# Optimization experiments

Hardware: AMD Instinct MI355X
Metric: run time of the kernel (lower is better)

## Reference

```python
import jax, jax.numpy as jnp
import numpy as np

VOCAB_SIZES = [100003, 100019, 100043, 100049, 100057, 100069, 100103, 100109,
               100129, 100151, 100153, 100169, 100183, 100189, 100193, 100207]
OFFSETS = np.cumsum([0] + VOCAB_SIZES[:-1]).astype(np.int32)  # per-head offsets into shared table
B, S, G, C = 2, 2048, 4, 2048        # batch, seq, hc_mult branches, base_emb_dim
H, DH = 16, 64                        # total hash heads, dim_per_head
ENGRAM_DIM = H * DH                   # 1024 = num_orders * dim_per_ngram
K, DIL = 4, 3                         # conv kernel_size, dilation = max_ngram_size


def setup_inputs() -> dict:
  key = jax.random.key(0)
  ks = jax.random.split(key, 8)
  total_vocab = sum(VOCAB_SIZES)
  return {
      "hidden_states": jax.random.normal(ks[0], (B, S, G, C), jnp.float32),
      "hash_input_ids": jax.random.randint(ks[1], (B, S, H), 0, min(VOCAB_SIZES), jnp.int32),
      "emb_table": jax.random.normal(ks[2], (total_vocab, DH), jnp.float32) * 0.02,
      "key_w": jax.random.normal(ks[3], (G, ENGRAM_DIM, C), jnp.float32) / np.sqrt(ENGRAM_DIM),
      "key_b": jnp.zeros((G, C), jnp.float32),
      "k_scale": jnp.ones((G, C), jnp.float32) + 0.02 * jax.random.normal(ks[4], (G, C), jnp.float32),
      "q_scale": jnp.ones((G, C), jnp.float32) + 0.02 * jax.random.normal(ks[5], (G, C), jnp.float32),
      "value_w": jax.random.normal(ks[6], (ENGRAM_DIM, C), jnp.float32) / np.sqrt(ENGRAM_DIM),
      "value_b": jnp.zeros((C,), jnp.float32),
      "conv_scale": jnp.ones((G, C), jnp.float32),
      "conv_w": jax.random.normal(ks[7], (K, G * C), jnp.float32) * 0.25,  # depthwise taps
  }


def _rmsnorm(x, scale, eps):
  var = jnp.mean(jnp.square(x), axis=-1, keepdims=True)
  return x * jax.lax.rsqrt(var + eps) * scale


def reference(hidden_states, hash_input_ids, emb_table, key_w, key_b,
              k_scale, q_scale, value_w, value_b, conv_scale, conv_w):
  # 1. Retrieve: offset-shifted multi-head embedding gather
  ids = hash_input_ids + jnp.asarray(OFFSETS)            # (B,S,H)
  emb = emb_table[ids].reshape(B, S, ENGRAM_DIM)         # (B,S,H*DH)
  # 2. Gate: per-branch key projections + RMSNorms, signed-sqrt sigmoid gate
  keys = jnp.einsum('bse,geo->bsgo', emb, key_w) + key_b  # (B,S,G,C)
  k = _rmsnorm(keys, k_scale, 1e-6)
  q = _rmsnorm(hidden_states, q_scale, 1e-6)
  qk = jnp.einsum('bsgc,bsgc->bsg', q, k) / jnp.sqrt(jnp.float32(C))
  gate_logits = jnp.sqrt(jnp.maximum(jnp.abs(qk), 1e-6)) * jnp.sign(qk)
  gates = jax.nn.sigmoid(gate_logits)                    # (B,S,G)
  value = emb @ value_w + value_b                        # (B,S,C)
  v = gates[..., None] * value[:, :, None, :]            # (B,S,G,C)
  # 3. Mix: ShortConv = SiLU(depthwise causal dilated Conv1D(RMSNorm(v)))
  xn = _rmsnorm(v, conv_scale, 1e-5).reshape(B, S, G * C)
  pad = (K - 1) * DIL                                    # causal left pad = 9
  xp = jnp.pad(xn, ((0, 0), (pad, 0), (0, 0)))
  y = sum(xp[:, j * DIL:j * DIL + S, :] * conv_w[j] for j in range(K))
  y = jax.nn.silu(y).reshape(B, S, G, C)
  return v + y
```

## Files before the change

### kernel.cpp

```cpp
#include <hip/hip_runtime.h>
#include <cstdint>
#include <cstddef>

typedef __attribute__((ext_vector_type(8))) __bf16 bf16x8;
typedef __attribute__((ext_vector_type(4))) float f32x4;
typedef __attribute__((ext_vector_type(4))) unsigned short u16x4;
typedef __attribute__((ext_vector_type(8))) unsigned short u16x8;

static constexpr int Bz = 2, Sz = 2048, Gz = 4, Cz = 2048;
static constexpr int Hh = 16, EDz = 1024;
static constexpr int Tz = Bz * Sz;
static constexpr int NALL = Gz * Cz + Cz;

__constant__ int OFF16[16] = {0, 100003, 200022, 300065, 400114, 500171, 600240,
                              700343, 800452, 900581, 1000732, 1100885, 1201054,
                              1301237, 1401426, 1501619};

__device__ __forceinline__ float bf2f(unsigned short s) {
  union { unsigned u; float f; } x; x.u = ((unsigned)s) << 16; return x.f;
}
__device__ __forceinline__ unsigned short f2bf(float f) {
  union { float f; unsigned u; } x; x.f = f;
  unsigned r = x.u + 0x7fff + ((x.u >> 16) & 1);
  return (unsigned short)(r >> 16);
}

__global__ __launch_bounds__(256) void k_prep(const float* __restrict__ key_w,
                                              const float* __restrict__ value_w,
                                              const float* __restrict__ table,
                                              const int* __restrict__ ids,
                                              unsigned short* __restrict__ Wt,
                                              unsigned short* __restrict__ emb,
                                              float* __restrict__ sums) {
  const int b = blockIdx.x;
  __shared__ float tile[32][33];
  if (b < 10240) {
    const int mat = b / 2048;
    const int inner = b - mat * 2048;
    const int ot = inner & 63, kt = inner >> 6;
    const float* src = (mat < 4) ? (key_w + (size_t)mat * EDz * Cz) : value_w;
    const int tx = threadIdx.x & 31, ty = threadIdx.x >> 5;
#pragma unroll
    for (int i = 0; i < 4; i++)
      tile[ty + i * 8][tx] = src[(size_t)(kt * 32 + ty + i * 8) * Cz + ot * 32 + tx];
    __syncthreads();
#pragma unroll
    for (int i = 0; i < 4; i++)
      Wt[(size_t)(mat * Cz + ot * 32 + ty + i * 8) * EDz + kt * 32 + tx] =
          f2bf(tile[tx][ty + i * 8]);
  } else if (b < 14336) {
    const int t = b - 10240;
    const int tid = threadIdx.x;
    const int h = tid >> 4;
    const int d = (tid & 15) * 4;
    const long row = (long)(ids[t * Hh + h] + OFF16[h]);
    f32x4 v = *reinterpret_cast<const f32x4*>(table + row * 64 + d);
    u16x4 o;
#pragma unroll
    for (int i = 0; i < 4; i++) o[i] = f2bf(v[i]);
    *reinterpret_cast<u16x4*>(emb + (size_t)t * EDz + tid * 4) = o;
  } else {
    const int i = (b - 14336) * 256 + threadIdx.x;
    if (i < 53248) sums[i] = 0.f;
  }
}

#define GEMM_BAR  asm volatile("s_barrier" ::: "memory")
#define GEMM_V4   asm volatile("s_waitcnt vmcnt(4)" ::: "memory")

__global__ __launch_bounds__(512, 2) void k_gemm8f(const unsigned short* __restrict__ A,
                                                   const unsigned short* __restrict__ Bw,
                                                   const float* __restrict__ hidden,
                                                   const float* __restrict__ key_b,
                                                   const float* __restrict__ value_b,
                                                   const float* __restrict__ q_scale,
                                                   const float* __restrict__ k_scale,
                                                   float* __restrict__ sums,
                                                   unsigned short* __restrict__ vbuf) {
  __shared__ unsigned short s_lds[65536];
  char* lds_c = (char*)s_lds;

  const int tid = threadIdx.x;
  const int wid = tid >> 6, lane = tid & 63;
  const int wr = wid >> 2, wc = wid & 3;

  const int bid = blockIdx.x;
  const int swz = (bid & 7) * 80 + (bid >> 3);
  const int bm = swz / 40, bn = swz % 40;
  const int m0 = bm * 256, n0 = bn * 256;

  int rq[2], kq[2];
#pragma unroll
  for (int q = 0; q < 2; q++) {
    int x = q * 8192 + wid * 1024 + lane * 16;
    int y = x ^ (((x >> 9) & 1) << 5);
    rq[q] = ((y >> 11) & 7) * 16 + ((y >> 6) & 15);
    kq[q] = ((y >> 10) & 1) * 32 + ((y >> 1) & 31);
  }
  const int rdb = (((lane & 15) << 6) + ((lane >> 4) << 4)) ^ (((lane >> 3) & 1) << 5);

  const unsigned short* Arow0 = A + (size_t)m0 * EDz;
  const unsigned short* Arow1 = A + (size_t)(m0 + 128) * EDz;
  const unsigned short* Brow0 = Bw + (size_t)n0 * EDz;
  const unsigned short* Brow1 = Bw + (size_t)(n0 + 128) * EDz;

  auto STAGE = [&](const unsigned short* grow, int ldsOff, int kt) {
#pragma unroll
    for (int q = 0; q < 2; q++) {
      const unsigned short* src = grow + (size_t)rq[q] * EDz + kt * 64 + kq[q];
      __builtin_amdgcn_global_load_lds(
          (const __attribute__((address_space(1))) void*)src,
          (__attribute__((address_space(3))) void*)(lds_c + ldsOff + q * 8192 + wid * 1024),
          16, 0, 0);
    }
  };

  f32x4 acc[8][4] = {};
  bf16x8 Af[4][2], Bl[2][2], Bh[2][2];

  auto RD_A = [&](int buf, int msel) {
    const char* p = lds_c + buf * 32768 + wr * 16384 + rdb;
#pragma unroll
    for (int m = 0; m < 4; m++)
#pragma unroll
      for (int ks = 0; ks < 2; ks++)
        Af[m][ks] = *reinterpret_cast<const bf16x8*>(p + (msel * 4 + m) * 2048 + ks * 1024);
  };
  auto RD_B = [&](int buf, int nsel, bf16x8 (&Bf)[2][2]) {
    const char* p = lds_c + 65536 + buf * 32768 + (wc >> 1) * 16384 + (wc & 1) * 8192 + rdb;
#pragma unroll
    for (int n = 0; n < 2; n++)
#pragma unroll
      for (int ks = 0; ks < 2; ks++)
        Bf[n][ks] = *reinterpret_cast<const bf16x8*>(p + (nsel * 2 + n) * 2048 + ks * 1024);
  };
  auto MM = [&](int msel, int nsel, bf16x8 (&Bf)[2][2]) {
    __builtin_amdgcn_s_setprio(1);
#pragma unroll
    for (int m = 0; m < 4; m++)
#pragma unroll
      for (int n = 0; n < 2; n++)
#pragma unroll
        for (int ks = 0; ks < 2; ks++)
          acc[msel * 4 + m][nsel * 2 + n] = __builtin_amdgcn_mfma_f32_16x16x32_bf16(
              Af[m][ks], Bf[n][ks], acc[msel * 4 + m][nsel * 2 + n], 0, 0, 0);
    __builtin_amdgcn_s_setprio(0);
  };

  STAGE(Arow0, 0,             0);
  STAGE(Arow1, 16384,         0);
  STAGE(Brow0, 65536,         0);
  STAGE(Brow1, 65536 + 16384, 0);
  STAGE(Brow0, 65536 + 32768,         1);
  STAGE(Brow1, 65536 + 32768 + 16384, 1);
  GEMM_V4;
  GEMM_BAR;

  for (int i = 0; i < 8; ++i) {
    const int o  = 2 * i + 1;
    const int t2 = (2 * i + 2 > 15) ? 15 : 2 * i + 2;
    const int t3 = (2 * i + 3 > 15) ? 15 : 2 * i + 3;
    RD_A(0, 0); RD_B(0, 0, Bl);
    STAGE(Arow0, 32768, o);
    GEMM_BAR; MM(0, 0, Bl); GEMM_BAR;
    RD_B(0, 1, Bh);
    STAGE(Arow1, 32768 + 16384, o);
    GEMM_BAR; MM(0, 1, Bh); GEMM_BAR;
    RD_A(0, 1);
    STAGE(Brow0, 65536, t2);
    GEMM_BAR; MM(1, 0, Bl); GEMM_BAR;
    STAGE(Brow1, 65536 + 16384, t2);
    GEMM_V4;
    GEMM_BAR; MM(1, 1, Bh); GEMM_BAR;
    RD_A(1, 0); RD_B(1, 0, Bl);
    STAGE(Arow0, 0, t2);
    GEMM_BAR; MM(0, 0, Bl); GEMM_BAR;
    RD_B(1, 1, Bh);
    STAGE(Arow1, 16384, t2);
    GEMM_BAR; MM(0, 1, Bh); GEMM_BAR;
    RD_A(1, 1);
    STAGE(Brow0, 65536 + 32768, t3);
    GEMM_BAR; MM(1, 0, Bl); GEMM_BAR;
    STAGE(Brow1, 65536 + 32768 + 16384, t3);
    GEMM_V4;
    GEMM_BAR; MM(1, 1, Bh); GEMM_BAR;
  }

  float* sum_q2  = sums;
  float* sum_k2  = sums + 16384;
  float* sum_qwk = sums + 32768;
  float* sum_v2  = sums + 49152;

  if (n0 < 8192) {
    const int g = n0 >> 11;
#pragma unroll
    for (int mrep = 0; mrep < 8; mrep++) {
      const int rowb = wr * 128 + mrep * 16 + (lane >> 4) * 4;
#pragma unroll
      for (int nrep = 0; nrep < 4; nrep++) {
        const int coll = wc * 64 + nrep * 16 + (lane & 15);
        const float kb = key_b[n0 + coll];
#pragma unroll
        for (int t = 0; t < 4; t++) {
          const int row = rowb + t;
          const int addr = (row * 512 + coll * 2) ^ ((row & 15) << 4);
          *reinterpret_cast<unsigned short*>(lds_c + addr) =
              f2bf(acc[mrep][nrep][t] + kb);
        }
      }
    }
    __syncthreads();
    const int wrow = wid * 32;
    const int lrow = lane >> 3;
    const int lsub = lane & 7;
#pragma unroll
    for (int rr = 0; rr < 4; rr++) {
      const int row = wrow + rr * 8 + lrow;
      const int grow = m0 + row;
      const float* hp = hidden + (size_t)grow * 8192 + n0;
      float a_k2 = 0.f, a_qwk = 0.f, a_q2 = 0.f;
#pragma unroll
      for (int c8 = 0; c8 < 4; c8++) {
        const int lc = c8 * 64 + lsub * 8;
        const int addr = (row * 512 + lc * 2) ^ ((row & 15) << 4);
        bf16x8 k8 = *reinterpret_cast<const bf16x8*>(lds_c + addr);
        f32x4 h0 = *reinterpret_cast<const f32x4*>(hp + lc);
        f32x4 h1 = *reinterpret_cast<const f32x4*>(hp + lc + 4);
        f32x4 qs0 = *reinterpret_cast<const f32x4*>(q_scale + n0 + lc);
        f32x4 qs1 = *reinterpret_cast<const f32x4*>(q_scale + n0 + lc + 4);
        f32x4 ks0 = *reinterpret_cast<const f32x4*>(k_scale + n0 + lc);
        f32x4 ks1 = *reinterpret_cast<const f32x4*>(k_scale + n0 + lc + 4);
#pragma unroll
        for (int i = 0; i < 8; i++) {
          const float kf = (float)k8[i];
          const float hf = (i < 4) ? h0[i] : h1[i - 4];
          const float wf = ((i < 4) ? qs0[i] : qs1[i - 4]) *
                           ((i < 4) ? ks0[i] : ks1[i - 4]);
          a_k2  += kf * kf;
          a_qwk += kf * hf * wf;
          a_q2  += hf * hf;
        }
      }
#pragma unroll
      for (int msk = 1; msk <= 4; msk <<= 1) {
        a_k2  += __shfl_xor(a_k2, msk);
        a_qwk += __shfl_xor(a_qwk, msk);
        a_q2  += __shfl_xor(a_q2, msk);
      }
      if (lsub == 0) {
        const int idx = grow * 4 + g;
        atomicAdd(&sum_k2[idx], a_k2);
        atomicAdd(&sum_qwk[idx], a_qwk);
        atomicAdd(&sum_q2[idx], a_q2);
      }
    }
  } else {
#pragma unroll
    for (int mrep = 0; mrep < 8; mrep++) {
      const int rowb = m0 + wr * 128 + mrep * 16 + (lane >> 4) * 4;
      float av2[4] = {0.f, 0.f, 0.f, 0.f};
#pragma unroll
      for (int nrep = 0; nrep < 4; nrep++) {
        const int vcol = n0 - 8192 + wc * 64 + nrep * 16 + (lane & 15);
        const float vb = value_b[vcol];
#pragma unroll
        for (int t = 0; t < 4; t++) {
          const float v = acc[mrep][nrep][t] + vb;
          av2[t] += v * v;
          vbuf[(size_t)(rowb + t) * 2048 + vcol] = f2bf(v);
        }
      }
#pragma unroll
      for (int t = 0; t < 4; t++) {
        float a = av2[t];
#pragma unroll
        for (int msk = 1; msk <= 8; msk <<= 1) a += __shfl_xor(a, msk);
        if ((lane & 15) == 0) atomicAdd(&sum_v2[rowb + t], a);
      }
    }
  }
}

__global__ __launch_bounds__(256) void k_conv(const unsigned short* __restrict__ vbuf,
                                              const float* __restrict__ sums,
                                              const float* __restrict__ conv_scale,
                                              const float* __restrict__ conv_w,
                                              float* __restrict__ out) {
  const int th = threadIdx.x;
  const int r = blockIdx.x % 3, seg = blockIdx.x / 3;
  const int bg = blockIdx.y;
  const int b = bg >> 2, g = bg & 3;
  const int c8 = th * 8;
  const int ch = g * Cz + c8;
  const int s_begin = seg * 64, s_end = s_begin + 64;

  __shared__ float g_lds[73], r_lds[73];
  if (th < 73) {
    const int s = s_begin - 9 + th;
    if (s >= 0) {
      const int t = b * Sz + s;
      const int idx = t * 4 + g;
      const float invC = 1.f / 2048.f;
      const float inv_sqrtC = 0.02209708691f;
      float rqv = rsqrtf(sums[idx] * invC + 1e-6f);
      float rkv = rsqrtf(sums[16384 + idx] * invC + 1e-6f);
      float qk = sums[32768 + idx] * rqv * rkv * inv_sqrtC;
      float l = sqrtf(fmaxf(fabsf(qk), 1e-6f));
      l = (qk < 0.f) ? -l : l;
      float gate = 1.f / (1.f + expf(-l));
      g_lds[th] = gate;
      r_lds[th] = rsqrtf(gate * gate * (sums[49152 + t] * invC) + 1e-5f);
    } else {
      g_lds[th] = 0.f; r_lds[th] = 0.f;
    }
  }
  __syncthreads();

  float cs[8], w0[8], w1[8], w2[8], w3[8];
#pragma unroll
  for (int q = 0; q < 2; q++) {
    f32x4 a = *reinterpret_cast<const f32x4*>(conv_scale + ch + q * 4);
    f32x4 t0 = *reinterpret_cast<const f32x4*>(conv_w + 0 * 8192 + ch + q * 4);
    f32x4 t1 = *reinterpret_cast<const f32x4*>(conv_w + 1 * 8192 + ch + q * 4);
    f32x4 t2 = *reinterpret_cast<const f32x4*>(conv_w + 2 * 8192 + ch + q * 4);
    f32x4 t3 = *reinterpret_cast<const f32x4*>(conv_w + 3 * 8192 + ch + q * 4);
#pragma unroll
    for (int i = 0; i < 4; i++) {
      cs[q * 4 + i] = a[i];
      w0[q * 4 + i] = t0[i]; w1[q * 4 + i] = t1[i];
      w2[q * 4 + i] = t2[i]; w3[q * 4 + i] = t3[i];
    }
  }

  const int s0 = s_begin + ((r - s_begin) % 3 + 3) % 3;

  float p1[8], p2[8], p3[8];
  auto ldxn = [&](int s, float* dst) {
    if (s < 0) {
#pragma unroll
      for (int i = 0; i < 8; i++) dst[i] = 0.f;
      return;
    }
    const int t = b * Sz + s;
    const int li = s - s_begin + 9;
    const float grs = g_lds[li] * r_lds[li];
    u16x8 raw = *reinterpret_cast<const u16x8*>(vbuf + (size_t)t * 2048 + c8);
#pragma unroll
    for (int i = 0; i < 8; i++) dst[i] = bf2f(raw[i]) * grs * cs[i];
  };
  ldxn(s0 - 3, p1); ldxn(s0 - 6, p2); ldxn(s0 - 9, p3);

  for (int s = s0; s < s_end; s += 3) {
    const int t = b * Sz + s;
    const int li = s - s_begin + 9;
    const float gate = g_lds[li];
    const float rsc = r_lds[li];
    u16x8 raw = *reinterpret_cast<const u16x8*>(vbuf + (size_t)t * 2048 + c8);
    f32x4 o0, o1;
#pragma unroll
    for (int i = 0; i < 8; i++) {
      float v = bf2f(raw[i]) * gate;
      float xn = v * rsc * cs[i];
      float y = w3[i] * xn + w2[i] * p1[i] + w1[i] * p2[i] + w0[i] * p3[i];
      float sy = y / (1.f + expf(-y));
      float ov = v + sy;
      if (i < 4) o0[i] = ov; else o1[i - 4] = ov;
      p3[i] = p2[i]; p2[i] = p1[i]; p1[i] = xn;
    }
    float* op = out + (size_t)t * (Gz * Cz) + ch;
    *reinterpret_cast<f32x4*>(op) = o0;
    *reinterpret_cast<f32x4*>(op + 4) = o1;
  }
}

extern "C" void kernel_launch(void* const* d_in, const int* in_sizes, int n_in,
                              void* d_out, int out_size, void* d_ws, size_t ws_size,
                              hipStream_t stream) {
  const float* hidden     = (const float*)d_in[0];
  const int*   hashids    = (const int*)d_in[1];
  const float* table      = (const float*)d_in[2];
  const float* key_w      = (const float*)d_in[3];
  const float* key_b      = (const float*)d_in[4];
  const float* k_scale    = (const float*)d_in[5];
  const float* q_scale    = (const float*)d_in[6];
  const float* value_w    = (const float*)d_in[7];
  const float* value_b    = (const float*)d_in[8];
  const float* conv_scale = (const float*)d_in[9];
  const float* conv_w     = (const float*)d_in[10];
  float* out = (float*)d_out;
  char* ws = (char*)d_ws;

  unsigned short* emb  = (unsigned short*)(ws + 0);
  unsigned short* Wt   = (unsigned short*)(ws + 8388608);
  unsigned short* vbuf = (unsigned short*)(ws + 29360128);
  float* sums  = (float*)(ws + 46137344);

  k_prep<<<dim3(14544), dim3(256), 0, stream>>>(key_w, value_w, table, hashids,
                                                Wt, emb, sums);
  k_gemm8f<<<dim3(640), dim3(512), 0, stream>>>(emb, Wt, hidden, key_b, value_b,
                                                q_scale, k_scale, sums, vbuf);
  k_conv<<<dim3(96, 8), dim3(256), 0, stream>>>(vbuf, sums, conv_scale, conv_w, out);
}
```

Before: 193.9 us.

## Share vbuf loads across branches in conv kernel and vectorize Wt transpose stores

The conv kernel now assigns each thread two channels across all four branches, so each bf16 value row is read once per token instead of once per branch (vbuf holds a single value shared by every branch). Blocks grow to 1024 threads and the grid shrinks to 96x2, with per-branch gate and rsqrt tables kept in LDS. The weight transpose in k_prep now writes four bf16 values per thread as one 8-byte store instead of scalar 2-byte stores. Trade-offs: fewer blocks and larger blocks may reduce occupancy and latency hiding, and output stores narrow from 16-byte to 8-byte vectors.

```diff
diff --git a/kernel.cpp b/kernel.cpp
--- a/kernel.cpp
+++ b/kernel.cpp
@@ -4,6 +4,8 @@
 
 typedef __attribute__((ext_vector_type(8))) __bf16 bf16x8;
 typedef __attribute__((ext_vector_type(4))) float f32x4;
+typedef __attribute__((ext_vector_type(2))) float f32x2;
+typedef __attribute__((ext_vector_type(2))) unsigned short u16x2;
 typedef __attribute__((ext_vector_type(4))) unsigned short u16x4;
 typedef __attribute__((ext_vector_type(8))) unsigned short u16x8;
 
@@ -44,10 +46,12 @@
     for (int i = 0; i < 4; i++)
       tile[ty + i * 8][tx] = src[(size_t)(kt * 32 + ty + i * 8) * Cz + ot * 32 + tx];
     __syncthreads();
-#pragma unroll
-    for (int i = 0; i < 4; i++)
-      Wt[(size_t)(mat * Cz + ot * 32 + ty + i * 8) * EDz + kt * 32 + tx] =
-          f2bf(tile[tx][ty + i * 8]);
+    const int nl = threadIdx.x >> 3, kq = threadIdx.x & 7;
+    u16x4 o;
+#pragma unroll
+    for (int c = 0; c < 4; c++) o[c] = f2bf(tile[kq * 4 + c][nl]);
+    *reinterpret_cast<u16x4*>(
+        &Wt[(size_t)(mat * Cz + ot * 32 + nl) * EDz + kt * 32 + kq * 4]) = o;
   } else if (b < 14336) {
     const int t = b - 10240;
     const int tid = threadIdx.x;
@@ -281,22 +285,21 @@
   }
 }
 
-__global__ __launch_bounds__(256) void k_conv(const unsigned short* __restrict__ vbuf,
-                                              const float* __restrict__ sums,
-                                              const float* __restrict__ conv_scale,
-                                              const float* __restrict__ conv_w,
-                                              float* __restrict__ out) {
+__global__ __launch_bounds__(1024, 4) void k_conv(const unsigned short* __restrict__ vbuf,
+                                                  const float* __restrict__ sums,
+                                                  const float* __restrict__ conv_scale,
+                                                  const float* __restrict__ conv_w,
+                                                  float* __restrict__ out) {
   const int th = threadIdx.x;
   const int r = blockIdx.x % 3, seg = blockIdx.x / 3;
-  const int bg = blockIdx.y;
-  const int b = bg >> 2, g = bg & 3;
-  const int c8 = th * 8;
-  const int ch = g * Cz + c8;
+  const int b = blockIdx.y;
+  const int c2 = th * 2;
   const int s_begin = seg * 64, s_end = s_begin + 64;
 
-  __shared__ float g_lds[73], r_lds[73];
-  if (th < 73) {
-    const int s = s_begin - 9 + th;
+  __shared__ float g_lds[4][73], r_lds[4][73];
+  if (th < 292) {
+    const int g = th / 73, j = th % 73;
+    const int s = s_begin - 9 + j;
     if (s >= 0) {
       const int t = b * Sz + s;
       const int idx = t * 4 + g;
@@ -308,68 +311,74 @@
       float l = sqrtf(fmaxf(fabsf(qk), 1e-6f));
       l = (qk < 0.f) ? -l : l;
       float gate = 1.f / (1.f + expf(-l));
-      g_lds[th] = gate;
-      r_lds[th] = rsqrtf(gate * gate * (sums[49152 + t] * invC) + 1e-5f);
+      g_lds[g][j] = gate;
+      r_lds[g][j] = rsqrtf(gate * gate * (sums[49152 + t] * invC) + 1e-5f);
     } else {
-      g_lds[th] = 0.f; r_lds[th] = 0.f;
+      g_lds[g][j] = 0.f; r_lds[g][j] = 0.f;
     }
   }
   __syncthreads();
 
-  float cs[8], w0[8], w1[8], w2[8], w3[8];
-#pragma unroll
-  for (int q = 0; q < 2; q++) {
-    f32x4 a = *reinterpret_cast<const f32x4*>(conv_scale + ch + q * 4);
-    f32x4 t0 = *reinterpret_cast<const f32x4*>(conv_w + 0 * 8192 + ch + q * 4);
-    f32x4 t1 = *reinterpret_cast<const f32x4*>(conv_w + 1 * 8192 + ch + q * 4);
-    f32x4 t2 = *reinterpret_cast<const f32x4*>(conv_w + 2 * 8192 + ch + q * 4);
-    f32x4 t3 = *reinterpret_cast<const f32x4*>(conv_w + 3 * 8192 + ch + q * 4);
-#pragma unroll
-    for (int i = 0; i < 4; i++) {
-      cs[q * 4 + i] = a[i];
-      w0[q * 4 + i] = t0[i]; w1[q * 4 + i] = t1[i];
-      w2[q * 4 + i] = t2[i]; w3[q * 4 + i] = t3[i];
+  float cs[4][2], w0[4][2], w1[4][2], w2[4][2], w3[4][2];
+#pragma unroll
+  for (int g = 0; g < 4; g++) {
+    const int ch = g * Cz + c2;
+    f32x2 a  = *reinterpret_cast<const f32x2*>(conv_scale + ch);
+    f32x2 t0 = *reinterpret_cast<const f32x2*>(conv_w + 0 * 8192 + ch);
+    f32x2 t1 = *reinterpret_cast<const f32x2*>(conv_w + 1 * 8192 + ch);
+    f32x2 t2 = *reinterpret_cast<const f32x2*>(conv_w + 2 * 8192 + ch);
+    f32x2 t3 = *reinterpret_cast<const f32x2*>(conv_w + 3 * 8192 + ch);
+#pragma unroll
+    for (int i = 0; i < 2; i++) {
+      cs[g][i] = a[i];
+      w0[g][i] = t0[i]; w1[g][i] = t1[i];
+      w2[g][i] = t2[i]; w3[g][i] = t3[i];
     }
   }
 
   const int s0 = s_begin + ((r - s_begin) % 3 + 3) % 3;
 
-  float p1[8], p2[8], p3[8];
-  auto ldxn = [&](int s, float* dst) {
+  float p1[4][2], p2[4][2], p3[4][2];
+  auto ldxn = [&](int s, float (*dst)[2]) {
     if (s < 0) {
 #pragma unroll
-      for (int i = 0; i < 8; i++) dst[i] = 0.f;
+      for (int g = 0; g < 4; g++) { dst[g][0] = 0.f; dst[g][1] = 0.f; }
       return;
     }
     const int t = b * Sz + s;
     const int li = s - s_begin + 9;
-    const float grs = g_lds[li] * r_lds[li];
-    u16x8 raw = *reinterpret_cast<const u16x8*>(vbuf + (size_t)t * 2048 + c8);
-#pragma unroll
-    for (int i = 0; i < 8; i++) dst[i] = bf2f(raw[i]) * grs * cs[i];
+    u16x2 raw = *reinterpret_cast<const u16x2*>(vbuf + (size_t)t * 2048 + c2);
+#pragma unroll
+    for (int g = 0; g < 4; g++) {
+      const float grs = g_lds[g][li] * r_lds[g][li];
+#pragma unroll
+      for (int i = 0; i < 2; i++) dst[g][i] = bf2f(raw[i]) * grs * cs[g][i];
+    }
   };
   ldxn(s0 - 3, p1); ldxn(s0 - 6, p2); ldxn(s0 - 9, p3);
 
   for (int s = s0; s < s_end; s += 3) {
     const int t = b * Sz + s;
     const int li = s - s_begin + 9;
-    const float gate = g_lds[li];
-    const float rsc = r_lds[li];
-    u16x8 raw = *reinterpret_cast<const u16x8*>(vbuf + (size_t)t * 2048 + c8);
-    f32x4 o0, o1;
-#pragma unroll
-    for (int i = 0; i < 8; i++) {
-      float v = bf2f(raw[i]) * gate;
-      float xn = v * rsc * cs[i];
-      float y = w3[i] * xn + w2[i] * p1[i] + w1[i] * p2[i] + w0[i] * p3[i];
-      float sy = y / (1.f + expf(-y));
-      float ov = v + sy;
-      if (i < 4) o0[i] = ov; else o1[i - 4] = ov;
-      p3[i] = p2[i]; p2[i] = p1[i]; p1[i] = xn;
-    }
-    float* op = out + (size_t)t * (Gz * Cz) + ch;
-    *reinterpret_cast<f32x4*>(op) = o0;
-    *reinterpret_cast<f32x4*>(op + 4) = o1;
+    u16x2 raw = *reinterpret_cast<const u16x2*>(vbuf + (size_t)t * 2048 + c2);
+    const float v0f = bf2f(raw[0]), v1f = bf2f(raw[1]);
+#pragma unroll
+    for (int g = 0; g < 4; g++) {
+      const float gate = g_lds[g][li];
+      const float rsc = r_lds[g][li];
+      f32x2 ov;
+#pragma unroll
+      for (int i = 0; i < 2; i++) {
+        const float v = ((i == 0) ? v0f : v1f) * gate;
+        const float xn = v * rsc * cs[g][i];
+        const float y = w3[g][i] * xn + w2[g][i] * p1[g][i] +
+                        w1[g][i] * p2[g][i] + w0[g][i] * p3[g][i];
+        const float sy = y / (1.f + expf(-y));
+        ov[i] = v + sy;
+        p3[g][i] = p2[g][i]; p2[g][i] = p1[g][i]; p1[g][i] = xn;
+      }
+      *reinterpret_cast<f32x2*>(out + (size_t)t * (Gz * Cz) + g * Cz + c2) = ov;
+    }
   }
 }
 
@@ -399,5 +408,5 @@
                                                 Wt, emb, sums);
   k_gemm8f<<<dim3(640), dim3(512), 0, stream>>>(emb, Wt, hidden, key_b, value_b,
                                                 q_scale, k_scale, sums, vbuf);
-  k_conv<<<dim3(96, 8), dim3(256), 0, stream>>>(vbuf, sums, conv_scale, conv_w, out);
-}
+  k_conv<<<dim3(96, 2), dim3(1024), 0, stream>>>(vbuf, sums, conv_scale, conv_w, out);
+}
```

Measured after the change: 205.4 us. +5.9%, slower.
